# Optimization experiments

Hardware: AMD Instinct MI355X
Metric: run time of the kernel (lower is better)

## Reference

```python
import jax, jax.numpy as jnp
import numpy as np

LOG1000 = 6.9077542789816375  # ln(1000)


def setup_inputs() -> dict:
    key = jax.random.key(0)
    kx, kp = jax.random.split(key)
    x = jax.random.normal(kx, (65536, 128), dtype=jnp.float32)
    points = jax.random.normal(kp, (2048, 128), dtype=jnp.float32)
    beta_raw = jnp.array([-3.5], dtype=jnp.float32)
    return {"x": x, "points": points, "beta_raw": beta_raw}


def reference(x, points, beta_raw):
    t1 = jnp.sum(x * x, axis=-1, keepdims=True)            # [N, 1]
    t2 = jnp.sum(points * points, axis=-1)[None, :]        # [1, P]
    t3 = 2.0 * jnp.einsum('nd,pd->np', x, points)          # [N, P]
    d2 = jnp.clip(t1 + t2 - t3, 0.0)
    min_d = jnp.min(d2, axis=-1)                           # [N]
    # translated sigmoid
    beta = jax.nn.softplus(beta_raw)                       # [1]
    alpha = -beta * LOG1000
    return jax.nn.sigmoid((min_d + alpha) / beta)
```

## Files before the change

### kernel.cpp

```cpp
#include <hip/hip_runtime.h>


#define NROWS 65536
#define NPTS  2048
#define DIMS  128
#define LOG1000F 6.9077542789816375f

typedef __attribute__((ext_vector_type(8))) int i32x8;
typedef __attribute__((ext_vector_type(4))) float f32x4;

union AFrag { int d[8]; i32x8 v; };
union BFrag { uint4 u4[2]; i32x8 v; };

__global__ __launch_bounds__(256) void prep_points_kernel(
    const float* __restrict__ pts, unsigned char* __restrict__ ptsf8,
    float* __restrict__ pnorm)
{
    int tid  = threadIdx.x;
    int lane = tid & 63;
    int w    = tid >> 6;
    int pt   = blockIdx.x * 4 + w;
    const float2 v = *reinterpret_cast<const float2*>(
        pts + (size_t)pt * DIMS + lane * 2);
    int pk = __builtin_amdgcn_cvt_pk_fp8_f32(v.x, v.y, 0, false);
    int T  = pt >> 4, pm = pt & 15;
    int q  = lane >> 4;
    int c  = (lane >> 3) & 1;
    int j  = (lane & 7) * 2;
    size_t dst = (size_t)((T * 2 + c) * 64 + q * 16 + pm) * 16 + j;
    *reinterpret_cast<unsigned short*>(ptsf8 + dst) =
        (unsigned short)(pk & 0xFFFF);
    float ss = v.x * v.x + v.y * v.y;
    ss += __shfl_xor(ss, 1, 64);
    ss += __shfl_xor(ss, 2, 64);
    ss += __shfl_xor(ss, 4, 64);
    ss += __shfl_xor(ss, 8, 64);
    ss += __shfl_xor(ss, 16, 64);
    ss += __shfl_xor(ss, 32, 64);
    if (lane == 0) pnorm[pt] = ss;
}

__global__ __launch_bounds__(256, 2) void distnet_main_kernel(
    const float* __restrict__ x, const unsigned char* __restrict__ ptsf8,
    const float* __restrict__ pnorm, const float* __restrict__ beta_raw,
    float* __restrict__ out)
{
    __shared__ __align__(16) float s_pn[NPTS];
    __shared__ __align__(16) int s_af[8][64][8];
    __shared__ float s_red[2][128];
    __shared__ float s_xn[128];

    int tid = threadIdx.x;
    {
        const float4* p4 = reinterpret_cast<const float4*>(pnorm);
        float4* d4 = reinterpret_cast<float4*>(s_pn);
        float4 a = p4[tid], b = p4[tid + 256];
        d4[tid]       = make_float4(-.5f*a.x, -.5f*a.y, -.5f*a.z, -.5f*a.w);
        d4[tid + 256] = make_float4(-.5f*b.x, -.5f*b.y, -.5f*b.z, -.5f*b.w);
    }

    int wid   = tid >> 6, lane = tid & 63;
    int m     = lane & 15, q = lane >> 4;
    int pairw = wid >> 1, half = wid & 1;
    int rbase0 = blockIdx.x * 128;

#pragma unroll
    for (int i = 0; i < 2; ++i) {
        int lt = wid * 2 + i;
        const float* xp = x + (size_t)(rbase0 + lt * 16 + m) * DIMS + q * 32;
        AFrag af;
        float s = 0.f;
#pragma unroll
        for (int d = 0; d < 8; ++d) {
            float4 v = *reinterpret_cast<const float4*>(xp + d * 4);
            int w0 = __builtin_amdgcn_cvt_pk_fp8_f32(v.x, v.y, 0, false);
            w0 = __builtin_amdgcn_cvt_pk_fp8_f32(v.z, v.w, w0, true);
            af.d[d] = w0;
            s += v.x * v.x + v.y * v.y + v.z * v.z + v.w * v.w;
        }
        s += __shfl_xor(s, 16, 64);
        s += __shfl_xor(s, 32, 64);
        if (q == 0) s_xn[lt * 16 + m] = s;
        *reinterpret_cast<i32x8*>(&s_af[lt][lane][0]) = af.v;
    }
    __syncthreads();

    AFrag afrag[4];
#pragma unroll
    for (int t = 0; t < 4; ++t)
        afrag[t].v = *reinterpret_cast<const i32x8*>(&s_af[pairw * 4 + t][lane][0]);

    float runmax[4][4];
#pragma unroll
    for (int t = 0; t < 4; ++t)
#pragma unroll
        for (int r = 0; r < 4; ++r) runmax[t][r] = -1e30f;

    const uint4* bsw = reinterpret_cast<const uint4*>(ptsf8);
    const int T0 = half * 32;

    BFrag bA, bB, bC, bD;
    float pnA, pnB, pnC, pnD;

#define LOADT(gT, buf, pnh) do {                       \
        buf.u4[0] = bsw[(gT) * 128 + lane];            \
        buf.u4[1] = bsw[(gT) * 128 + 64 + lane];       \
        pnh = s_pn[(gT) * 16 + m];                     \
    } while (0)

    auto compute = [&](const BFrag& buf, float pnh) {
#pragma unroll
        for (int t = 0; t < 4; ++t) {
            f32x4 acc = {pnh, pnh, pnh, pnh};
            acc = __builtin_amdgcn_mfma_scale_f32_16x16x128_f8f6f4(
                afrag[t].v, buf.v, acc, 0, 0, 0, 0x7F7F7F7F, 0, 0x7F7F7F7F);
#pragma unroll
            for (int r = 0; r < 4; ++r)
                runmax[t][r] = fmaxf(runmax[t][r], acc[r]);
        }
    };

    LOADT(T0 + 0, bA, pnA);
    LOADT(T0 + 1, bB, pnB);
    LOADT(T0 + 2, bC, pnC);
    LOADT(T0 + 3, bD, pnD);
#pragma unroll 1
    for (int T = 0; T < 92; T += 4) {
        compute(bA, pnA);
        LOADT(T0 + T + 4, bA, pnA);
        compute(bB, pnB);
        LOADT(T0 + T + 5, bB, pnB);
        compute(bC, pnC);
        LOADT(T0 + T + 6, bC, pnC);
        compute(bD, pnD);
        LOADT(T0 + T + 7, bD, pnD);
    }
    compute(bA, pnA);
    compute(bB, pnB);
    compute(bC, pnC);
    compute(bD, pnD);
#undef LOADT

#pragma unroll
    for (int t = 0; t < 4; ++t) {
#pragma unroll
        for (int r = 0; r < 4; ++r) {
            float v = runmax[t][r];
            v = fmaxf(v, __shfl_xor(v, 1, 64));
            v = fmaxf(v, __shfl_xor(v, 2, 64));
            v = fmaxf(v, __shfl_xor(v, 4, 64));
            v = fmaxf(v, __shfl_xor(v, 8, 64));
            if (m == 0)
                s_red[half][pairw * 64 + t * 16 + q * 4 + r] = v;
        }
    }
    __syncthreads();

    if (tid < 128) {
        float vmax  = fmaxf(s_red[0][tid], s_red[1][tid]);
        float d2    = fmaxf(fmaf(-2.f, vmax, s_xn[tid]), 0.f);
        float br    = beta_raw[0];
        float beta  = log1pf(expf(br));
        float alpha = -beta * LOG1000F;
        float z     = (d2 + alpha) / beta;
        out[(size_t)blockIdx.x * 128 + tid] = 1.f / (1.f + expf(-z));
    }
}

extern "C" void kernel_launch(void* const* d_in, const int* in_sizes, int n_in,
                              void* d_out, int out_size, void* d_ws, size_t ws_size,
                              hipStream_t stream) {
    const float* x        = (const float*)d_in[0];
    const float* pts      = (const float*)d_in[1];
    const float* beta_raw = (const float*)d_in[2];
    float* out            = (float*)d_out;

    unsigned char* ptsf8 = (unsigned char*)d_ws;
    float* pnorm = (float*)((char*)d_ws + (size_t)NPTS * DIMS);

    prep_points_kernel<<<NPTS / 4, 256, 0, stream>>>(pts, ptsf8, pnorm);
    distnet_main_kernel<<<NROWS / 128, 256, 0, stream>>>(x, ptsf8, pnorm,
                                                         beta_raw, out);
}
```

Baseline: 97.00 us.

## Split point range across four waves per row group with 512-thread blocks

The main kernel now runs 512 threads per block. Eight waves form two row groups, and each group splits the 128 point tiles four ways instead of two, with a four-way max reduction through shared memory at the end. The first B-fragment global loads are issued before the barrier so they overlap the x conversion. This is meant to raise wave-level parallelism and hide load latency, at the cost of more register and LDS pressure and an extra reduction stage.

Result: faster. 94.47 us (-2.6%).

```diff
diff --git a/kernel.cpp b/kernel.cpp
--- a/kernel.cpp
+++ b/kernel.cpp
@@ -40,33 +40,31 @@
     if (lane == 0) pnorm[pt] = ss;
 }
 
-__global__ __launch_bounds__(256, 2) void distnet_main_kernel(
+__global__ __launch_bounds__(512, 2) void distnet_main_kernel(
     const float* __restrict__ x, const unsigned char* __restrict__ ptsf8,
     const float* __restrict__ pnorm, const float* __restrict__ beta_raw,
     float* __restrict__ out)
 {
     __shared__ __align__(16) float s_pn[NPTS];
     __shared__ __align__(16) int s_af[8][64][8];
-    __shared__ float s_red[2][128];
+    __shared__ float s_red[4][128];
     __shared__ float s_xn[128];
 
     int tid = threadIdx.x;
     {
         const float4* p4 = reinterpret_cast<const float4*>(pnorm);
-        float4* d4 = reinterpret_cast<float4*>(s_pn);
-        float4 a = p4[tid], b = p4[tid + 256];
-        d4[tid]       = make_float4(-.5f*a.x, -.5f*a.y, -.5f*a.z, -.5f*a.w);
-        d4[tid + 256] = make_float4(-.5f*b.x, -.5f*b.y, -.5f*b.z, -.5f*b.w);
+        float4 a = p4[tid];
+        reinterpret_cast<float4*>(s_pn)[tid] =
+            make_float4(-.5f*a.x, -.5f*a.y, -.5f*a.z, -.5f*a.w);
     }
 
-    int wid   = tid >> 6, lane = tid & 63;
-    int m     = lane & 15, q = lane >> 4;
-    int pairw = wid >> 1, half = wid & 1;
+    int wid  = tid >> 6, lane = tid & 63;
+    int m    = lane & 15, q = lane >> 4;
+    int g    = wid >> 2, c = wid & 3;
     int rbase0 = blockIdx.x * 128;
 
-#pragma unroll
-    for (int i = 0; i < 2; ++i) {
-        int lt = wid * 2 + i;
+    {
+        int lt = wid;
         const float* xp = x + (size_t)(rbase0 + lt * 16 + m) * DIMS + q * 32;
         AFrag af;
         float s = 0.f;
@@ -83,24 +81,36 @@
         if (q == 0) s_xn[lt * 16 + m] = s;
         *reinterpret_cast<i32x8*>(&s_af[lt][lane][0]) = af.v;
     }
+
+    const uint4* bsw = reinterpret_cast<const uint4*>(ptsf8);
+    const int T0 = c * 32;
+    BFrag bA, bB, bC, bD;
+    bA.u4[0] = bsw[(T0 + 0) * 128 + lane];
+    bA.u4[1] = bsw[(T0 + 0) * 128 + 64 + lane];
+    bB.u4[0] = bsw[(T0 + 1) * 128 + lane];
+    bB.u4[1] = bsw[(T0 + 1) * 128 + 64 + lane];
+    bC.u4[0] = bsw[(T0 + 2) * 128 + lane];
+    bC.u4[1] = bsw[(T0 + 2) * 128 + 64 + lane];
+    bD.u4[0] = bsw[(T0 + 3) * 128 + lane];
+    bD.u4[1] = bsw[(T0 + 3) * 128 + 64 + lane];
+
     __syncthreads();
 
     AFrag afrag[4];
 #pragma unroll
     for (int t = 0; t < 4; ++t)
-        afrag[t].v = *reinterpret_cast<const i32x8*>(&s_af[pairw * 4 + t][lane][0]);
+        afrag[t].v = *reinterpret_cast<const i32x8*>(&s_af[g * 4 + t][lane][0]);
+
+    float pnA = s_pn[(T0 + 0) * 16 + m];
+    float pnB = s_pn[(T0 + 1) * 16 + m];
+    float pnC = s_pn[(T0 + 2) * 16 + m];
+    float pnD = s_pn[(T0 + 3) * 16 + m];
 
     float runmax[4][4];
 #pragma unroll
     for (int t = 0; t < 4; ++t)
 #pragma unroll
         for (int r = 0; r < 4; ++r) runmax[t][r] = -1e30f;
-
-    const uint4* bsw = reinterpret_cast<const uint4*>(ptsf8);
-    const int T0 = half * 32;
-
-    BFrag bA, bB, bC, bD;
-    float pnA, pnB, pnC, pnD;
 
 #define LOADT(gT, buf, pnh) do {                       \
         buf.u4[0] = bsw[(gT) * 128 + lane];            \
@@ -120,12 +130,8 @@
         }
     };
 
-    LOADT(T0 + 0, bA, pnA);
-    LOADT(T0 + 1, bB, pnB);
-    LOADT(T0 + 2, bC, pnC);
-    LOADT(T0 + 3, bD, pnD);
 #pragma unroll 1
-    for (int T = 0; T < 92; T += 4) {
+    for (int T = 0; T < 28; T += 4) {
         compute(bA, pnA);
         LOADT(T0 + T + 4, bA, pnA);
         compute(bB, pnB);
@@ -151,13 +157,14 @@
             v = fmaxf(v, __shfl_xor(v, 4, 64));
             v = fmaxf(v, __shfl_xor(v, 8, 64));
             if (m == 0)
-                s_red[half][pairw * 64 + t * 16 + q * 4 + r] = v;
+                s_red[c][g * 64 + t * 16 + q * 4 + r] = v;
         }
     }
     __syncthreads();
 
     if (tid < 128) {
-        float vmax  = fmaxf(s_red[0][tid], s_red[1][tid]);
+        float vmax  = fmaxf(fmaxf(s_red[0][tid], s_red[1][tid]),
+                            fmaxf(s_red[2][tid], s_red[3][tid]));
         float d2    = fmaxf(fmaf(-2.f, vmax, s_xn[tid]), 0.f);
         float br    = beta_raw[0];
         float beta  = log1pf(expf(br));
@@ -179,6 +186,6 @@
     float* pnorm = (float*)((char*)d_ws + (size_t)NPTS * DIMS);
 
     prep_points_kernel<<<NPTS / 4, 256, 0, stream>>>(pts, ptsf8, pnorm);
-    distnet_main_kernel<<<NROWS / 128, 256, 0, stream>>>(x, ptsf8, pnorm,
+    distnet_main_kernel<<<NROWS / 128, 512, 0, stream>>>(x, ptsf8, pnorm,
                                                          beta_raw, out);
 }
```
